# Kernel optimization log

Measured on AMD Instinct MI355X. Metric: run time of the kernel, lower is better.

The kernel has to match this reference:

```python
import jax, jax.numpy as jnp
import numpy as np
import math


def pos_enc_3d(h, w, d, c):
    # Faithful PositionalEncoding3D: channels = ceil(c/6)*2 (made even), sin/cos per axis.
    cpe = int(np.ceil(c / 6) * 2)
    if cpe % 2:
        cpe += 1
    inv_freq = 1.0 / (10000.0 ** (np.arange(0, cpe, 2, dtype=np.float32) / cpe))

    def axis_emb(n):
        s = np.arange(n, dtype=np.float32)[:, None] * inv_freq  # (n, cpe//2)
        return np.concatenate([np.sin(s), np.cos(s)], axis=-1)  # (n, cpe)

    ex = np.broadcast_to(axis_emb(h)[:, None, None, :], (h, w, d, cpe))
    ey = np.broadcast_to(axis_emb(w)[None, :, None, :], (h, w, d, cpe))
    ez = np.broadcast_to(axis_emb(d)[None, None, :, :], (h, w, d, cpe))
    emb = np.concatenate([ex, ey, ez], axis=-1)[..., :c]  # (h,w,d,c)
    return jnp.asarray(np.transpose(emb, (3, 0, 1, 2)))  # (c,h,w,d)


def conv3d(x, w, b):
    # x: (b,c,h,w,d), w: (o,i,3,3,3), padding=1
    y = jax.lax.conv_general_dilated(
        x, w, window_strides=(1, 1, 1), padding=[(1, 1)] * 3,
        dimension_numbers=('NCHWD', 'OIHWD', 'NCHWD'))
    return y + b[None, :, None, None, None]


def setup_inputs() -> dict:
    key = jax.random.key(0)
    ks = jax.random.split(key, 12)
    B, C, H, W, D = 2, 64, 16, 16, 16
    C8 = C // 8
    s_emb = 1.0 / math.sqrt(C)
    s_conv = 1.0 / math.sqrt(C * 27)
    return {
        'x': jax.random.normal(ks[0], (B, C, H, W, D), dtype=jnp.float32),
        'Wq': jax.random.normal(ks[1], (C, C), dtype=jnp.float32) * s_emb,
        'Wk': jax.random.normal(ks[2], (C, C), dtype=jnp.float32) * s_emb,
        'Wv': jax.random.normal(ks[3], (C, C), dtype=jnp.float32) * s_emb,
        'qw': jax.random.normal(ks[4], (C8, C, 3, 3, 3), dtype=jnp.float32) * s_conv,
        'qb': jax.random.normal(ks[5], (C8,), dtype=jnp.float32) * 0.01,
        'kw': jax.random.normal(ks[6], (C8, C, 3, 3, 3), dtype=jnp.float32) * s_conv,
        'kb': jax.random.normal(ks[7], (C8,), dtype=jnp.float32) * 0.01,
        'vw': jax.random.normal(ks[8], (C, C, 3, 3, 3), dtype=jnp.float32) * s_conv,
        'vb': jax.random.normal(ks[9], (C,), dtype=jnp.float32) * 0.01,
        'lam1': jax.random.normal(ks[10], (1,), dtype=jnp.float32) * 0.5,
        'lam2': jax.random.normal(ks[11], (1,), dtype=jnp.float32) * 0.5,
    }


def reference(x, Wq, Wk, Wv, qw, qb, kw, kb, vw, vb, lam1, lam2):
    b, c, h, w, d = x.shape
    n = h * w * d
    # NOTE: torch code does `x += pe` in-place inside SelfAttention, so the
    # PE-added x is also what GSA and the residual see.
    pe = pos_enc_3d(h, w, d, c)  # (c,h,w,d)
    x_pe = x + pe[None]

    # ---- SelfAttention (TSA) ----
    tok = x_pe.reshape(b, c, n).transpose(0, 2, 1)  # (b,n,c)
    Q = jnp.einsum('bnc,cd->bnd', tok, Wq)
    K = jnp.einsum('bnc,cd->bnd', tok, Wk)
    V = jnp.einsum('bnc,cd->bnd', tok, Wv)
    A = jax.nn.softmax(jnp.einsum('bic,bjc->bij', Q, K) / math.sqrt(c), axis=-1)
    tsa = jnp.einsum('bij,bjc->bic', A, V).transpose(0, 2, 1).reshape(b, c, h, w, d)

    # ---- GlobalSpatialAttention (GSA) ----
    M = conv3d(x_pe, qw, qb).reshape(b, c // 8, n)   # (b,c/8,n)
    Nk = conv3d(x_pe, kw, kb).reshape(b, c // 8, n)  # (b,c/8,n)
    Wv_ = conv3d(x_pe, vw, vb).reshape(b, c, n)      # (b,c,n)
    Bm = jax.nn.softmax(jnp.einsum('bci,bcj->bij', M, Nk), axis=-1)  # (b,n,n)
    gsa = jnp.einsum('bcj,bij->bci', Wv_, Bm).reshape(b, c, h, w, d)

    return lam1[0] * tsa + lam2[0] * gsa + x_pe
```

## Files before the change

### kernel.cpp

```cpp
#include <hip/hip_runtime.h>
#include <math.h>

#define BB 2
#define CC 64
#define NN 4096
#define CN (CC*NN)
#define NJ 8
#define NT ((NN/NJ)/64)

#define LOG2E 1.4426950408889634f
#define QSCALE 0.18033688011112042f
#define RESC_THR 8.0f

#define XT_ROWS 4097
#define WQKV_OFF (27*80*64)

typedef __attribute__((ext_vector_type(8))) short short8;
typedef __attribute__((ext_vector_type(4))) float float4v;
typedef unsigned short ushortT;

__device__ __forceinline__ ushortT f2bf(float x) {
    union { float f; unsigned u; } v; v.f = x;
    unsigned r = v.u + 0x7FFF + ((v.u >> 16) & 1);
    return (ushortT)(r >> 16);
}
__device__ __forceinline__ float bf2f(short s) {
    union { unsigned u; float f; } v;
    v.u = ((unsigned)(unsigned short)s) << 16;
    return v.f;
}
__device__ __forceinline__ unsigned pk2(float a, float b) {
    unsigned ua = __float_as_uint(a) + 0x8000u;
    unsigned ub = __float_as_uint(b) + 0x8000u;
    return __builtin_amdgcn_perm(ub, ua, 0x07060302);
}

__device__ __forceinline__ float pe_tab_val(int c, int pos) {
    int c2 = (c < 22) ? c : (c < 44) ? (c - 22) : (c - 44);
    int is_cos = (c2 >= 11);
    int k = c2 - (is_cos ? 11 : 0);
    float freq = exp2f(-1.2079738526863135f * (float)k);
    float arg = (float)pos * freq;
    return is_cos ? cosf(arg) : sinf(arg);
}

__global__ __launch_bounds__(256) void k_pre(const float* __restrict__ x,
                                             const float* __restrict__ qw,
                                             const float* __restrict__ kw,
                                             const float* __restrict__ vw,
                                             const float* __restrict__ Wq,
                                             const float* __restrict__ Wk,
                                             const float* __restrict__ Wv,
                                             float* __restrict__ xpe,
                                             ushortT* __restrict__ Xt,
                                             ushortT* __restrict__ Wr,
                                             ushortT* __restrict__ Qb,
                                             ushortT* __restrict__ Kb,
                                             ushortT* __restrict__ Vtb) {
    int blk = blockIdx.x, t = threadIdx.x;
    if (blk < 128) {
        __shared__ float sT[64][65];
        __shared__ float sPE[64][17];
        __shared__ ushortT sWt[64][72];
        __shared__ ushortT sVt[64][72];
        int b = blk >> 6, pos0 = (blk & 63) * 64;

        #pragma unroll
        for (int k = 0; k < 4; k++) {
            int e = t + k * 256;
            int c = e >> 4, coord = e & 15;
            sPE[c][coord] = pe_tab_val(c, coord);
        }
        __syncthreads();

        int pin = t & 63, cg0 = t >> 6;
        #pragma unroll
        for (int pass = 0; pass < 16; pass++) {
            int c = pass * 4 + cg0;
            int pos = pos0 + pin;
            int coord = (c < 22) ? (pos >> 8) : (c < 44) ? ((pos >> 4) & 15) : (pos & 15);
            size_t gi = (size_t)(b * 64 + c) * NN + pos;
            float v = x[gi] + sPE[c][coord];
            xpe[gi] = v;
            sT[c][pin] = v;
        }
        __syncthreads();

        {
            int po = t & 63, cg = t >> 6;
            #pragma unroll
            for (int half = 0; half < 2; half++) {
                int c0 = cg * 8 + half * 32;
                union { ushortT u[8]; short8 s; } pk_;
                #pragma unroll
                for (int e = 0; e < 8; e++) pk_.u[e] = f2bf(sT[c0 + e][po]);
                *(short8*)(Xt + ((size_t)b * XT_ROWS + pos0 + po + 1) * 64 + c0) = pk_.s;
            }
            if ((blk & 63) == 0 && t < 64)
                Xt[((size_t)b * XT_ROWS) * 64 + t] = 0;
        }

        int w = t >> 6, l = t & 63, lane15 = l & 15, q = l >> 4;
        int row = w * 16 + lane15;
        short8 a0, a1;
        {
            union { ushortT u[8]; short8 s; } t0, t1;
            #pragma unroll
            for (int e = 0; e < 8; e++) {
                t0.u[e] = f2bf(sT[q * 8 + e][row]);
                t1.u[e] = f2bf(sT[32 + q * 8 + e][row]);
            }
            a0 = t0.s; a1 = t1.s;
        }

        #pragma unroll
        for (int mat = 0; mat < 3; mat++) {
            const float* Wm = (mat == 0) ? Wq : (mat == 1) ? Wk : Wv;
            float sc = (mat == 0) ? QSCALE : 1.f;
            __syncthreads();
            #pragma unroll
            for (int p = 0; p < 4; p++) {
                int idx = t + p * 256;
                int c = idx >> 4, d4 = (idx & 15) * 4;
                float4 wv = *(const float4*)&Wm[c * 64 + d4];
                sWt[d4 + 0][c] = f2bf(wv.x * sc);
                sWt[d4 + 1][c] = f2bf(wv.y * sc);
                sWt[d4 + 2][c] = f2bf(wv.z * sc);
                sWt[d4 + 3][c] = f2bf(wv.w * sc);
            }
            __syncthreads();

            float4v acc[4];
            #pragma unroll
            for (int cg = 0; cg < 4; cg++) {
                const ushortT* wrow = &sWt[cg * 16 + lane15][0];
                short8 b0 = *(const short8*)(wrow + q * 8);
                short8 b1 = *(const short8*)(wrow + 32 + q * 8);
                float4v a = (float4v)0.f;
                a = __builtin_amdgcn_mfma_f32_16x16x32_bf16(a0, b0, a, 0, 0, 0);
                a = __builtin_amdgcn_mfma_f32_16x16x32_bf16(a1, b1, a, 0, 0, 0);
                acc[cg] = a;
            }
            if (mat < 2) {
                #pragma unroll
                for (int cg = 0; cg < 4; cg++)
                    #pragma unroll
                    for (int r = 0; r < 4; r++)
                        sVt[w * 16 + q * 4 + r][cg * 16 + lane15] = f2bf(acc[cg][r]);
                __syncthreads();
                ushortT* o = (mat == 0) ? Qb : Kb;
                int pl = t >> 2, sg = t & 3;
                short8 v0 = *(const short8*)&sVt[pl][sg * 16];
                short8 v1 = *(const short8*)&sVt[pl][sg * 16 + 8];
                size_t bq = ((size_t)(b * NN + pos0 + pl)) * 64 + sg * 16;
                *(short8*)(o + bq) = v0;
                *(short8*)(o + bq + 8) = v1;
            } else {
                #pragma unroll
                for (int cg = 0; cg < 4; cg++)
                    #pragma unroll
                    for (int r = 0; r < 4; r++)
                        sVt[cg * 16 + lane15][w * 16 + q * 4 + r] = f2bf(acc[cg][r]);
                __syncthreads();
                int c2 = t >> 2, seg = t & 3;
                short8 v0 = *(const short8*)&sVt[c2][seg * 16];
                short8 v1 = *(const short8*)&sVt[c2][seg * 16 + 8];
                size_t base = ((size_t)(b * 64 + c2)) * NN + pos0 + seg * 16;
                *(short8*)(Vtb + base) = v0;
                *(short8*)(Vtb + base + 8) = v1;
            }
        }
    } else {
        int idx = (blk - 128) * 256 + t;
        if (idx < WQKV_OFF) {
            int ic = idx & 63;
            int oc = (idx >> 6) % 80;
            int tap = idx / 5120;
            float v;
            if (oc < 8)       v = qw[(oc * 64 + ic) * 27 + tap] * LOG2E;
            else if (oc < 16) v = kw[((oc - 8) * 64 + ic) * 27 + tap];
            else              v = vw[((oc - 16) * 64 + ic) * 27 + tap];
            Wr[idx] = f2bf(v);
        }
    }
}

template<int IS_TSA>
__device__ __forceinline__ void stage_load(short8* kst, short8* vst,
                                           const ushortT* __restrict__ Km,
                                           const ushortT* __restrict__ Vt,
                                           int b, int jb, int t) {
    if (IS_TSA) {
        #pragma unroll
        for (int ps = 0; ps < 2; ps++) {
            int idx = ps * 256 + t, j = idx >> 3, g = idx & 7;
            kst[ps] = *(const short8*)(Km + ((size_t)(b * NN + jb + j)) * 64 + g * 8);
        }
    } else {
        if (t < 64)
            kst[0] = *(const short8*)(Km + ((size_t)(b * NN + jb + t)) * 8);
    }
    #pragma unroll
    for (int ps = 0; ps < 2; ps++) {
        int idx = ps * 256 + t, c = idx >> 3, gj = idx & 7;
        vst[ps] = *(const short8*)(Vt + ((size_t)(b * 64 + c)) * NN + jb + gj * 8);
    }
}

template<int IS_TSA>
__device__ __forceinline__ void stage_write(const short8* kst, const short8* vst,
                                            ushortT* sK, ushortT* sV, int t) {
    if (IS_TSA) {
        #pragma unroll
        for (int ps = 0; ps < 2; ps++) {
            int idx = ps * 256 + t, j = idx >> 3, g = idx & 7;
            *(short8*)(sK + j * 64 + ((g ^ (j & 7)) * 8)) = kst[ps];
        }
    } else {
        if (t < 64)
            *(short8*)(sK + t * 64 + ((t & 7) * 8)) = kst[0];
    }
    #pragma unroll
    for (int ps = 0; ps < 2; ps++) {
        int idx = ps * 256 + t, c = idx >> 3, gj = idx & 7;
        *(short8*)(sV + c * 64 + ((gj ^ (c & 7)) * 8)) = vst[ps];
    }
}

template<int IS_TSA>
__device__ __forceinline__ void flash_body(int it, int jc, int b, int t,
                                           const ushortT* __restrict__ Qm,
                                           const ushortT* __restrict__ Km,
                                           const ushortT* __restrict__ Vt,
                                           float* __restrict__ pM,
                                           float* __restrict__ pL,
                                           ushortT* __restrict__ pAcc,
                                           ushortT* __restrict__ sKb,
                                           ushortT* __restrict__ sVb,
                                           ushortT* __restrict__ sPall) {
    constexpr int KCH = IS_TSA ? 2 : 1;
    constexpr int DQ  = IS_TSA ? 64 : 8;
    int w = t >> 6, l = t & 63;
    int lane15 = l & 15, q = l >> 4;
    int i0a = it * 128 + w * 16;
    ushortT* myP = sPall + w * (16 * 64);

    short8 qf[2][KCH];
    #pragma unroll
    for (int si = 0; si < 2; si++) {
        const ushortT* qrow = Qm + ((size_t)(b * NN + i0a + si * 64 + lane15)) * DQ;
        if (IS_TSA) {
            qf[si][0] = *(const short8*)(qrow + q * 8);
            qf[si][1] = *(const short8*)(qrow + 32 + q * 8);
        } else {
            short8 z = (short8)0;
            if (q == 0) z = *(const short8*)qrow;
            qf[si][0] = z;
        }
    }

    float m_run[2] = {-3e38f, -3e38f}, Lacc[2] = {0.f, 0.f};
    float4v O[2][4];
    #pragma unroll
    for (int si = 0; si < 2; si++)
        #pragma unroll
        for (int cs = 0; cs < 4; cs++) O[si][cs] = (float4v)0.f;

    const int jbase0 = jc * (NN / NJ);

    short8 kst[2], vst[2];
    stage_load<IS_TSA>(kst, vst, Km, Vt, b, jbase0, t);
    stage_write<IS_TSA>(kst, vst, sKb, sVb, t);
    __syncthreads();

    for (int jt = 0; jt < NT; jt++) {
        int cur = jt & 1;
        ushortT* cK = sKb + cur * 4096;
        ushortT* cV = sVb + cur * 4096;
        bool more = (jt + 1 < NT);

        if (more) stage_load<IS_TSA>(kst, vst, Km, Vt, b, jbase0 + (jt + 1) * 64, t);

        short8 kf[4][KCH];
        #pragma unroll
        for (int sub = 0; sub < 4; sub++) {
            int jr = sub * 16 + lane15;
            if (IS_TSA) {
                kf[sub][0] = *(const short8*)(cK + jr * 64 + (((0 * 4 + q) ^ (lane15 & 7)) * 8));
                kf[sub][1] = *(const short8*)(cK + jr * 64 + (((1 * 4 + q) ^ (lane15 & 7)) * 8));
            } else {
                short8 z = (short8)0;
                if (q == 0) z = *(const short8*)(cK + jr * 64 + ((lane15 & 7) * 8));
                kf[sub][0] = z;
            }
        }

        float4v s[2][4];
        #pragma unroll
        for (int si = 0; si < 2; si++)
            #pragma unroll
            for (int sub = 0; sub < 4; sub++) {
                float4v acc = (float4v)0.f;
                #pragma unroll
                for (int kc = 0; kc < KCH; kc++)
                    acc = __builtin_amdgcn_mfma_f32_16x16x32_bf16(kf[sub][kc], qf[si][kc], acc, 0, 0, 0);
                s[si][sub] = acc;
            }

        short8 va[4], vbf[4];
        #pragma unroll
        for (int sub = 0; sub < 4; sub++) {
            int cr = sub * 16 + lane15;
            va[sub]  = *(const short8*)(cV + cr * 64 + ((q ^ (lane15 & 7)) * 8));
            vbf[sub] = *(const short8*)(cV + cr * 64 + (((4 + q) ^ (lane15 & 7)) * 8));
        }

        #pragma unroll
        for (int si = 0; si < 2; si++) {
            float tmax = fmaxf(fmaxf(fmaxf(s[si][0][0], s[si][0][1]), fmaxf(s[si][0][2], s[si][0][3])),
                               fmaxf(fmaxf(s[si][1][0], s[si][1][1]), fmaxf(s[si][1][2], s[si][1][3])));
            float tmax2 = fmaxf(fmaxf(fmaxf(s[si][2][0], s[si][2][1]), fmaxf(s[si][2][2], s[si][2][3])),
                                fmaxf(fmaxf(s[si][3][0], s[si][3][1]), fmaxf(s[si][3][2], s[si][3][3])));
            tmax = fmaxf(tmax, tmax2);
            tmax = fmaxf(tmax, __shfl_xor(tmax, 16));
            tmax = fmaxf(tmax, __shfl_xor(tmax, 32));

            if (!__all(tmax <= m_run[si] + RESC_THR)) {
                float mnew = fmaxf(m_run[si], tmax);
                float corr = exp2f(m_run[si] - mnew);
                Lacc[si] *= corr;
                float c0 = __shfl(corr, q * 4 + 0);
                float c1 = __shfl(corr, q * 4 + 1);
                float c2 = __shfl(corr, q * 4 + 2);
                float c3 = __shfl(corr, q * 4 + 3);
                #pragma unroll
                for (int cs = 0; cs < 4; cs++) {
                    O[si][cs][0] *= c0; O[si][cs][1] *= c1;
                    O[si][cs][2] *= c2; O[si][cs][3] *= c3;
                }
                m_run[si] = mnew;
            }
            float mcur = m_run[si];

            #pragma unroll
            for (int sub = 0; sub < 4; sub++) {
                float p0 = exp2f(s[si][sub][0] - mcur);
                float p1 = exp2f(s[si][sub][1] - mcur);
                float p2 = exp2f(s[si][sub][2] - mcur);
                float p3 = exp2f(s[si][sub][3] - mcur);
                Lacc[si] += (p0 + p1) + (p2 + p3);
                unsigned lo = pk2(p0, p1), hi = pk2(p2, p3);
                int g = sub * 2 + (q >> 1);
                unsigned* wp = (unsigned*)(myP + lane15 * 64 + ((g ^ (lane15 & 7)) * 8) + (q & 1) * 4);
                wp[0] = lo; wp[1] = hi;
            }

            short8 pf0 = *(const short8*)(myP + lane15 * 64 + (((0 * 4 + q) ^ (lane15 & 7)) * 8));
            short8 pf1 = *(const short8*)(myP + lane15 * 64 + (((1 * 4 + q) ^ (lane15 & 7)) * 8));

            #pragma unroll
            for (int sub = 0; sub < 4; sub++) {
                O[si][sub] = __builtin_amdgcn_mfma_f32_16x16x32_bf16(pf0, va[sub], O[si][sub], 0, 0, 0);
                O[si][sub] = __builtin_amdgcn_mfma_f32_16x16x32_bf16(pf1, vbf[sub], O[si][sub], 0, 0, 0);
            }
        }

        if (more)
            stage_write<IS_TSA>(kst, vst, sKb + (cur ^ 1) * 4096, sVb + (cur ^ 1) * 4096, t);
        __syncthreads();
    }

    #pragma unroll
    for (int si = 0; si < 2; si++) {
        size_t base = (size_t)(b * NJ + jc) * NN + i0a + si * 64;
        float Ls = Lacc[si];
        Ls += __shfl_xor(Ls, 16);
        Ls += __shfl_xor(Ls, 32);
        if (q == 0) {
            pL[base + lane15] = Ls;
            pM[base + lane15] = m_run[si];
        }
        #pragma unroll
        for (int cs = 0; cs < 4; cs++) {
            int g = cs * 2 + (lane15 >> 3);
            #pragma unroll
            for (int r = 0; r < 4; r++) {
                int rr = q * 4 + r;
                myP[rr * 64 + ((g ^ (rr & 7)) * 8) + (lane15 & 7)] = f2bf(O[si][cs][r]);
            }
        }
        int rrow = l >> 2, rs2 = (l & 3) * 2;
        short8 ov0 = *(const short8*)(myP + rrow * 64 + ((rs2 ^ (rrow & 7)) * 8));
        short8 ov1 = *(const short8*)(myP + rrow * 64 + (((rs2 + 1) ^ (rrow & 7)) * 8));
        size_t gb = (base + rrow) * 64 + (l & 3) * 16;
        *(short8*)(pAcc + gb) = ov0;
        *(short8*)(pAcc + gb + 8) = ov1;
    }
}

__device__ __forceinline__ void reduce_set(const float* __restrict__ pM,
                                           const float* __restrict__ pL,
                                           const ushortT* __restrict__ pAcc,
                                           int b, int n, int seg, float* v) {
    float mv[NJ], M = -3e38f;
    #pragma unroll
    for (int jcc = 0; jcc < NJ; jcc++) {
        mv[jcc] = pM[(size_t)(b * NJ + jcc) * NN + n];
        M = fmaxf(M, mv[jcc]);
    }
    float L = 0.f;
    #pragma unroll
    for (int e = 0; e < 8; e++) v[e] = 0.f;
    #pragma unroll
    for (int jcc = 0; jcc < NJ; jcc++) {
        size_t rb = (size_t)(b * NJ + jcc) * NN + n;
        float wgt = exp2f(mv[jcc] - M);
        L += pL[rb] * wgt;
        short8 x0 = *(const short8*)(pAcc + rb * 64 + seg * 8);
        #pragma unroll
        for (int e = 0; e < 8; e++) v[e] += wgt * bf2f(x0[e]);
    }
    float invL = 1.f / L;
    #pragma unroll
    for (int e = 0; e < 8; e++) v[e] *= invL;
}

__global__ __launch_bounds__(256, 3) void k_tsacv(const ushortT* __restrict__ Qb,
                                                  const ushortT* __restrict__ Kb,
                                                  const ushortT* __restrict__ Vtb,
                                                  const ushortT* __restrict__ Xt,
                                                  const ushortT* __restrict__ Wr,
                                                  const float* __restrict__ qb,
                                                  const float* __restrict__ kb,
                                                  const float* __restrict__ vb,
                                                  ushortT* __restrict__ Mt,
                                                  ushortT* __restrict__ Nt,
                                                  ushortT* __restrict__ Wvt,
                                                  float* __restrict__ pMt, float* __restrict__ pLt,
                                                  ushortT* __restrict__ pAccT) {
    __shared__ ushortT sm[20480];
    int bx = blockIdx.x, t = threadIdx.x;
    if (bx >= 128) {
        int fb = bx - 128;
        int it = fb & 31, jc = (fb >> 5) & 7, b = fb >> 8;
        flash_body<1>(it, jc, b, t, Qb, Kb, Vtb, pMt, pLt, pAccT,
                      sm, sm + 8192, sm + 16384);
    } else {
        int cv = bx;
        int tile = cv & 63, b = cv >> 6;
        int w = t >> 6, l = t & 63, lane15 = l & 15, q = l >> 4;
        int pos0 = tile * 64 + w * 16;
        const ushortT* xb = Xt + (size_t)b * XT_ROWS * 64;
        int pos = pos0 + lane15;
        int dz = pos & 15, wy = (pos >> 4) & 15, hx = pos >> 8;

        ushortT* sW = sm;

        float4v accA[5], accB[5];
        #pragma unroll
        for (int o = 0; o < 5; o++) { accA[o] = (float4v)0.f; accB[o] = (float4v)0.f; }

        short8 ws[3];
        auto ldW = [&](int tap) {
            #pragma unroll
            for (int c3 = 0; c3 < 3; c3++) {
                int idx = t + c3 * 256;
                if (idx < 640)
                    ws[c3] = *(const short8*)(Wr + (size_t)tap * 5120 + idx * 8);
            }
        };
        auto wrW = [&](ushortT* buf) {
            #pragma unroll
            for (int c3 = 0; c3 < 3; c3++) {
                int idx = t + c3 * 256;
                if (idx < 640) {
                    int row = idx >> 3, g = idx & 7;
                    *(short8*)(buf + row * 64 + ((g ^ (row & 7)) * 8)) = ws[c3];
                }
            }
        };
        short8 xc0, xc1, xn0, xn1;
        auto ldX = [&](int tap, short8& o0, short8& o1) {
            int dh = tap / 9 - 1, dw = (tap / 3) % 3 - 1, dd = tap % 3 - 1;
            int shift = dh * 256 + dw * 16 + dd;
            bool ok = ((unsigned)(hx + dh) < 16u) &&
                      ((unsigned)(wy + dw) < 16u) &&
                      ((unsigned)(dz + dd) < 16u);
            int row = ok ? (pos + shift + 1) : 0;
            const ushortT* xrow = xb + (size_t)row * 64 + q * 8;
            o0 = *(const short8*)xrow;
            o1 = *(const short8*)(xrow + 32);
        };

        ldW(0);
        ldX(0, xc0, xc1);
        wrW(sW);
        __syncthreads();

        #pragma unroll
        for (int tap = 0; tap < 27; tap++) {
            ushortT* cW = sW + (tap & 1) * 5120;
            bool more = (tap + 1 < 27);

            if (more) { ldW(tap + 1); ldX(tap + 1, xn0, xn1); }

            #pragma unroll
            for (int o = 0; o < 5; o++) {
                int wr2 = o * 16 + lane15;
                short8 a0 = *(const short8*)(cW + wr2 * 64 + ((q ^ (lane15 & 7)) * 8));
                short8 a1 = *(const short8*)(cW + wr2 * 64 + (((4 + q) ^ (lane15 & 7)) * 8));
                accA[o] = __builtin_amdgcn_mfma_f32_16x16x32_bf16(a0, xc0, accA[o], 0, 0, 0);
                accB[o] = __builtin_amdgcn_mfma_f32_16x16x32_bf16(a1, xc1, accB[o], 0, 0, 0);
            }

            if (more) wrW(sW + ((tap + 1) & 1) * 5120);
            __syncthreads();
            xc0 = xn0; xc1 = xn1;
        }

        #pragma unroll
        for (int o = 0; o < 5; o++) {
            float4v accT = accA[o] + accB[o];
            if (o == 0) {
                #pragma unroll
                for (int r = 0; r < 4; r++) {
                    int ol = q * 4 + r;
                    float v = accT[r];
                    if (ol < 8)
                        Mt[((size_t)(b * NN + pos)) * 8 + ol] = f2bf(v + qb[ol] * LOG2E);
                    else
                        Nt[((size_t)(b * NN + pos)) * 8 + (ol - 8)] = f2bf(v + kb[ol - 8]);
                }
            } else {
                #pragma unroll
                for (int r = 0; r < 4; r++) {
                    int oc = (o - 1) * 16 + q * 4 + r;
                    Wvt[((size_t)(b * 64 + oc)) * NN + pos] = f2bf(accT[r] + vb[oc]);
                }
            }
        }
    }
}

__global__ __launch_bounds__(256, 3) void k_gsa(const ushortT* __restrict__ Mtb,
                                                const ushortT* __restrict__ Ntb,
                                                const ushortT* __restrict__ Wvtb,
                                                float* __restrict__ pMg, float* __restrict__ pLg,
                                                ushortT* __restrict__ pAccG,
                                                const float* __restrict__ pMt,
                                                const float* __restrict__ pLt,
                                                const ushortT* __restrict__ pAccT,
                                                const float* __restrict__ xpe,
                                                const float* __restrict__ lam1,
                                                float* __restrict__ out) {
    __shared__ ushortT sm[20480];
    int bx = blockIdx.x, t = threadIdx.x;
    if (bx < 512) {
        int it = bx & 31, jc = (bx >> 5) & 7, b = bx >> 8;
        flash_body<0>(it, jc, b, t, Mtb, Ntb, Wvtb, pMg, pLg, pAccG,
                      sm, sm + 8192, sm + 16384);
    } else {
        int rb = bx - 512;
        int b = rb >> 7, n0 = (rb & 127) * 32;
        float (*sT_)[65] = (float(*)[65])sm;
        int pp = t >> 3, seg = t & 7, n = n0 + pp;

        float vt[8];
        reduce_set(pMt, pLt, pAccT, b, n, seg, vt);
        #pragma unroll
        for (int e = 0; e < 8; e++) sT_[pp][seg * 8 + e] = vt[e];
        __syncthreads();

        int c = t >> 2, ns = (t & 3) * 8;
        float la1 = lam1[0];
        size_t ob = ((size_t)(b * 64 + c)) * NN + n0 + ns;
        const float* xp = xpe + ob;
        #pragma unroll
        for (int j = 0; j < 8; j += 4) {
            float4 ov;
            ov.x = la1 * sT_[ns + j + 0][c] + xp[j + 0];
            ov.y = la1 * sT_[ns + j + 1][c] + xp[j + 1];
            ov.z = la1 * sT_[ns + j + 2][c] + xp[j + 2];
            ov.w = la1 * sT_[ns + j + 3][c] + xp[j + 3];
            *(float4*)(out + ob + j) = ov;
        }
    }
}

__global__ __launch_bounds__(256) void k_reduce_g(const float* __restrict__ pMg,
                                                  const float* __restrict__ pLg,
                                                  const ushortT* __restrict__ pAccG,
                                                  const float* __restrict__ lam2,
                                                  float* __restrict__ out) {
    __shared__ float sG[32][65];
    int t = threadIdx.x;
    int b = blockIdx.y;
    int n0 = blockIdx.x * 32;
    int pp = t >> 3, seg = t & 7;
    int n = n0 + pp;

    float vg[8];
    reduce_set(pMg, pLg, pAccG, b, n, seg, vg);
    #pragma unroll
    for (int e = 0; e < 8; e++) sG[pp][seg * 8 + e] = vg[e];
    __syncthreads();

    int c = t >> 2, ns = (t & 3) * 8;
    float la2 = lam2[0];
    size_t ob = ((size_t)(b * 64 + c)) * NN + n0 + ns;
    #pragma unroll
    for (int j = 0; j < 8; j += 4) {
        float4 cur = *(const float4*)(out + ob + j);
        cur.x += la2 * sG[ns + j + 0][c];
        cur.y += la2 * sG[ns + j + 1][c];
        cur.z += la2 * sG[ns + j + 2][c];
        cur.w += la2 * sG[ns + j + 3][c];
        *(float4*)(out + ob + j) = cur;
    }
}

extern "C" void kernel_launch(void* const* d_in, const int* in_sizes, int n_in,
                              void* d_out, int out_size, void* d_ws, size_t ws_size,
                              hipStream_t stream) {
    const float* x    = (const float*)d_in[0];
    const float* Wq   = (const float*)d_in[1];
    const float* Wk   = (const float*)d_in[2];
    const float* Wv   = (const float*)d_in[3];
    const float* qw   = (const float*)d_in[4];
    const float* qb   = (const float*)d_in[5];
    const float* kw   = (const float*)d_in[6];
    const float* kb   = (const float*)d_in[7];
    const float* vw   = (const float*)d_in[8];
    const float* vb   = (const float*)d_in[9];
    const float* lam1 = (const float*)d_in[10];
    const float* lam2 = (const float*)d_in[11];
    float* out = (float*)d_out;

    char* W = (char*)d_ws;
    float*   xpe   = (float*)(W);
    ushortT* Qb    = (ushortT*)(W + (2u << 20));
    ushortT* Kb    = (ushortT*)(W + (3u << 20));
    ushortT* Vtb   = (ushortT*)(W + (4u << 20));
    ushortT* Mtb   = (ushortT*)(W + (5u << 20));
    ushortT* Ntb   = (ushortT*)(W + (5u << 20) + (1u << 17));
    ushortT* Wvtb  = (ushortT*)(W + (5u << 20) + (2u << 17));
    ushortT* Xt    = (ushortT*)(W + (6u << 20) + (2u << 17));
    ushortT* Wr    = (ushortT*)(W + (7u << 20) + (1u << 19));
    float*   pLt   = (float*)(W + (8u << 20));
    float*   pLg   = (float*)(W + (8u << 20) + (1u << 18));
    float*   pMt   = (float*)(W + (8u << 20) + (2u << 18));
    float*   pMg   = (float*)(W + (8u << 20) + (3u << 18));
    ushortT* pAccT = (ushortT*)(W + (9u << 20));
    ushortT* pAccG = (ushortT*)(W + (17u << 20));

    k_pre<<<dim3(128 + WQKV_OFF / 256), dim3(256), 0, stream>>>(
        x, qw, kw, vw, Wq, Wk, Wv, xpe, Xt, Wr, Qb, Kb, Vtb);
    k_tsacv<<<dim3(128 + 32 * NJ * BB), dim3(256), 0, stream>>>(
        Qb, Kb, Vtb, Xt, Wr, qb, kb, vb, Mtb, Ntb, Wvtb, pMt, pLt, pAccT);
    k_gsa<<<dim3(512 + 256), dim3(256), 0, stream>>>(
        Mtb, Ntb, Wvtb, pMg, pLg, pAccG, pMt, pLt, pAccT, xpe, lam1, out);
    k_reduce_g<<<dim3(NN / 32, BB), dim3(256), 0, stream>>>(
        pMg, pLg, pAccG, lam2, out);
}
```

Measured before the change: 131.7 us.

## Fuse final split-K reduction into GSA kernel via last-block atomic counter

Removes the separate k_reduce_g launch and the extra TSA-reduce blocks. Each GSA flash block now bumps an atomic counter per (batch, row tile), and the last of the NJ column-chunk blocks to finish combines both the TSA and GSA partial results and writes the output in one pass. The counter is reset in k_pre. A trailing __syncthreads in the flash loop is also dropped on the final iteration. The intent is to save a kernel launch and a read-modify-write of the output, at the cost of serialising the reduction onto the last-arriving blocks.

```diff
diff --git a/kernel.cpp b/kernel.cpp
--- a/kernel.cpp
+++ b/kernel.cpp
@@ -56,7 +56,8 @@
                                              ushortT* __restrict__ Wr,
                                              ushortT* __restrict__ Qb,
                                              ushortT* __restrict__ Kb,
-                                             ushortT* __restrict__ Vtb) {
+                                             ushortT* __restrict__ Vtb,
+                                             int* __restrict__ cnt) {
     int blk = blockIdx.x, t = threadIdx.x;
     if (blk < 128) {
         __shared__ float sT[64][65];
@@ -171,6 +172,7 @@
             }
         }
     } else {
+        if (blk == 128 && t < 64) cnt[t] = 0;
         int idx = (blk - 128) * 256 + t;
         if (idx < WQKV_OFF) {
             int ic = idx & 63;
@@ -365,9 +367,10 @@
             }
         }
 
-        if (more)
+        if (more) {
             stage_write<IS_TSA>(kst, vst, sKb + (cur ^ 1) * 4096, sVb + (cur ^ 1) * 4096, t);
-        __syncthreads();
+            __syncthreads();
+        }
     }
 
     #pragma unroll
@@ -552,70 +555,49 @@
                                                 const ushortT* __restrict__ pAccT,
                                                 const float* __restrict__ xpe,
                                                 const float* __restrict__ lam1,
+                                                const float* __restrict__ lam2,
+                                                int* __restrict__ cnt,
                                                 float* __restrict__ out) {
     __shared__ ushortT sm[20480];
+    __shared__ int sLast;
     int bx = blockIdx.x, t = threadIdx.x;
-    if (bx < 512) {
-        int it = bx & 31, jc = (bx >> 5) & 7, b = bx >> 8;
-        flash_body<0>(it, jc, b, t, Mtb, Ntb, Wvtb, pMg, pLg, pAccG,
-                      sm, sm + 8192, sm + 16384);
-    } else {
-        int rb = bx - 512;
-        int b = rb >> 7, n0 = (rb & 127) * 32;
-        float (*sT_)[65] = (float(*)[65])sm;
-        int pp = t >> 3, seg = t & 7, n = n0 + pp;
-
-        float vt[8];
-        reduce_set(pMt, pLt, pAccT, b, n, seg, vt);
-        #pragma unroll
-        for (int e = 0; e < 8; e++) sT_[pp][seg * 8 + e] = vt[e];
+    int it = bx & 31, jc = (bx >> 5) & 7, b = bx >> 8;
+
+    flash_body<0>(it, jc, b, t, Mtb, Ntb, Wvtb, pMg, pLg, pAccG,
+                  sm, sm + 8192, sm + 16384);
+
+    __threadfence();
+    __syncthreads();
+    if (t == 0) sLast = (atomicAdd(&cnt[b * 32 + it], 1) == NJ - 1) ? 1 : 0;
+    __syncthreads();
+    if (!sLast) return;
+    __threadfence();
+
+    float (*sRed)[65] = (float(*)[65])sm;
+    float la1 = lam1[0], la2 = lam2[0];
+    int pp = t >> 3, seg = t & 7;
+    int c = t >> 2, ns = (t & 3) * 8;
+    for (int pass = 0; pass < 4; pass++) {
+        int n0 = it * 128 + pass * 32;
+        float vt[8], vg[8];
+        reduce_set(pMt, pLt, pAccT, b, n0 + pp, seg, vt);
+        reduce_set(pMg, pLg, pAccG, b, n0 + pp, seg, vg);
+        #pragma unroll
+        for (int e = 0; e < 8; e++)
+            sRed[pp][seg * 8 + e] = la1 * vt[e] + la2 * vg[e];
         __syncthreads();
-
-        int c = t >> 2, ns = (t & 3) * 8;
-        float la1 = lam1[0];
         size_t ob = ((size_t)(b * 64 + c)) * NN + n0 + ns;
         const float* xp = xpe + ob;
         #pragma unroll
         for (int j = 0; j < 8; j += 4) {
             float4 ov;
-            ov.x = la1 * sT_[ns + j + 0][c] + xp[j + 0];
-            ov.y = la1 * sT_[ns + j + 1][c] + xp[j + 1];
-            ov.z = la1 * sT_[ns + j + 2][c] + xp[j + 2];
-            ov.w = la1 * sT_[ns + j + 3][c] + xp[j + 3];
+            ov.x = sRed[ns + j + 0][c] + xp[j + 0];
+            ov.y = sRed[ns + j + 1][c] + xp[j + 1];
+            ov.z = sRed[ns + j + 2][c] + xp[j + 2];
+            ov.w = sRed[ns + j + 3][c] + xp[j + 3];
             *(float4*)(out + ob + j) = ov;
         }
-    }
-}
-
-__global__ __launch_bounds__(256) void k_reduce_g(const float* __restrict__ pMg,
-                                                  const float* __restrict__ pLg,
-                                                  const ushortT* __restrict__ pAccG,
-                                                  const float* __restrict__ lam2,
-                                                  float* __restrict__ out) {
-    __shared__ float sG[32][65];
-    int t = threadIdx.x;
-    int b = blockIdx.y;
-    int n0 = blockIdx.x * 32;
-    int pp = t >> 3, seg = t & 7;
-    int n = n0 + pp;
-
-    float vg[8];
-    reduce_set(pMg, pLg, pAccG, b, n, seg, vg);
-    #pragma unroll
-    for (int e = 0; e < 8; e++) sG[pp][seg * 8 + e] = vg[e];
-    __syncthreads();
-
-    int c = t >> 2, ns = (t & 3) * 8;
-    float la2 = lam2[0];
-    size_t ob = ((size_t)(b * 64 + c)) * NN + n0 + ns;
-    #pragma unroll
-    for (int j = 0; j < 8; j += 4) {
-        float4 cur = *(const float4*)(out + ob + j);
-        cur.x += la2 * sG[ns + j + 0][c];
-        cur.y += la2 * sG[ns + j + 1][c];
-        cur.z += la2 * sG[ns + j + 2][c];
-        cur.w += la2 * sG[ns + j + 3][c];
-        *(float4*)(out + ob + j) = cur;
+        __syncthreads();
     }
 }
 
@@ -652,13 +634,12 @@
     float*   pMg   = (float*)(W + (8u << 20) + (3u << 18));
     ushortT* pAccT = (ushortT*)(W + (9u << 20));
     ushortT* pAccG = (ushortT*)(W + (17u << 20));
+    int*     cnt   = (int*)(W + (25u << 20));
 
     k_pre<<<dim3(128 + WQKV_OFF / 256), dim3(256), 0, stream>>>(
-        x, qw, kw, vw, Wq, Wk, Wv, xpe, Xt, Wr, Qb, Kb, Vtb);
+        x, qw, kw, vw, Wq, Wk, Wv, xpe, Xt, Wr, Qb, Kb, Vtb, cnt);
     k_tsacv<<<dim3(128 + 32 * NJ * BB), dim3(256), 0, stream>>>(
         Qb, Kb, Vtb, Xt, Wr, qb, kb, vb, Mtb, Ntb, Wvtb, pMt, pLt, pAccT);
-    k_gsa<<<dim3(512 + 256), dim3(256), 0, stream>>>(
-        Mtb, Ntb, Wvtb, pMg, pLg, pAccG, pMt, pLt, pAccT, xpe, lam1, out);
-    k_reduce_g<<<dim3(NN / 32, BB), dim3(256), 0, stream>>>(
-        pMg, pLg, pAccG, lam2, out);
-}
+    k_gsa<<<dim3(512), dim3(256), 0, stream>>>(
+        Mtb, Ntb, Wvtb, pMg, pLg, pAccG, pMt, pLt, pAccT, xpe, lam1, lam2, cnt, out);
+}
```

Result: slower. 220.2 us (+67.2%).
